# Optimization experiments

Measured on AMD Instinct MI355X. Metric: run time of the kernel, lower is better.

Reference implementation:

```python
import jax, jax.numpy as jnp
import numpy as np


def _generate_fitpack_knots(x, k):
    # FITPACK-style knots: k+1 copies of x[0], k+1 copies of x[-1],
    # interior knots are length-k moving averages of x[1:-1].
    n = x.shape[0]
    n_interior = n - k - 1  # number of interior knots
    win_sum = x[1:1 + n_interior]
    for j in range(1, k):  # k is a small static int (e.g. 3)
        win_sum = win_sum + x[1 + j:1 + j + n_interior]
    interior = win_sum / k
    head = jnp.full((k + 1,), x[0], dtype=x.dtype)
    tail = jnp.full((k + 1,), x[-1], dtype=x.dtype)
    return jnp.concatenate([head, interior, tail])


def _safe_div(num, den):
    # torch.nan_to_num_(num/den): 0/0 -> 0, x/0 -> 0
    den_safe = jnp.where(den == 0, jnp.ones_like(den), den)
    return jnp.where(den == 0, jnp.zeros_like(num), num / den_safe)


def _bspline_basis_natural(x, k, t):
    n = x.shape[0]
    m = t.shape[0] - k - 1
    xc = x[:, None]  # [n, 1]
    # zeroth-order basis: indicator of knot interval, with boundary fixes
    b = ((t[None, :m] <= xc) & (xc < t[None, 1:m + 1])).astype(x.dtype)
    b = b.at[:, 0].set(jnp.where(x < t[1], jnp.ones_like(x), b[:, 0]))
    b = b.at[:, -1].set(jnp.where(x >= t[-2], jnp.ones_like(x), b[:, -1]))
    zeros_col = jnp.zeros((n, 1), dtype=x.dtype)
    # de Boor recursion over degree d = 1..k (k is static and small)
    for d in range(1, k + 1):
        L = _safe_div(xc - t[None, :m], (t[d:m + d] - t[:m])[None, :])
        R = _safe_div(t[None, d + 1:m + d + 1] - xc,
                      (t[d + 1:m + d + 1] - t[1:m + 1])[None, :])
        b_shift = jnp.concatenate([b[:, 1:], zeros_col], axis=1)
        b = L * b + R * b_shift
    return b  # [n, m]


def setup_inputs() -> dict:
    key = jax.random.key(0)
    N = 4096
    x = jnp.sort(jax.random.uniform(key, (N,), dtype=jnp.float32) * 10.0)
    s = jnp.asarray(1e-3, dtype=jnp.float32)
    return {"x": x, "s": s, "k": 3}


def reference(x, s, k):
    knots = _generate_fitpack_knots(x, k)
    basis_matrix = _bspline_basis_natural(x, k, knots)  # [n, m]
    m = basis_matrix.shape[-1]
    B_T_B = basis_matrix.T @ basis_matrix + s * jnp.eye(m, dtype=basis_matrix.dtype)
    return (knots, basis_matrix, B_T_B)
```

## Files before the change

### kernel.cpp

```cpp
#include <hip/hip_runtime.h>

#define K 3

__device__ __forceinline__ float tfun(const float* __restrict__ x, int j, int N) {
    if (j <= K) return x[0];
    if (j >= N) return x[N - 1];
    return (x[j - 3] + x[j - 2] + x[j - 1]) / 3.0f;
}

__global__ void k1_basis(const float* __restrict__ x, float* __restrict__ out_knots,
                         float* __restrict__ vals, int* __restrict__ j0arr, int N) {
    int i = blockIdx.x * blockDim.x + threadIdx.x;
    if (i >= N) return;
    int nk = N + K + 1;

    out_knots[i] = tfun(x, i, N);
    if (i < nk - N) out_knots[N + i] = x[N - 1];

    float xi = x[i];
    int lo = 0, hi = nk;
    while (lo < hi) { int mid = (lo + hi) >> 1; if (tfun(x, mid, N) <= xi) lo = mid + 1; else hi = mid; }
    int j0 = lo - 1;
    if (j0 > N - 1) j0 = N - 1;
    if (j0 < K) j0 = K;
    int c0 = j0 - K;

    float b[K + 2];
    #pragma unroll
    for (int w = 0; w < K + 2; ++w) b[w] = 0.f;
    b[K] = 1.f;

    #pragma unroll
    for (int d = 1; d <= K; ++d) {
        float nb[K + 1];
        #pragma unroll
        for (int w = 0; w <= K; ++w) {
            int j = c0 + w;
            float tj   = tfun(x, j, N);
            float tjd  = tfun(x, j + d, N);
            float tj1  = tfun(x, j + 1, N);
            float tjd1 = tfun(x, j + d + 1, N);
            float denL = tjd - tj;
            float L = (denL == 0.f) ? 0.f : (xi - tj) / denL;
            float denR = tjd1 - tj1;
            float R = (denR == 0.f) ? 0.f : (tjd1 - xi) / denR;
            nb[w] = L * b[w] + R * b[w + 1];
        }
        #pragma unroll
        for (int w = 0; w <= K; ++w) b[w] = nb[w];
    }

    j0arr[i] = j0;
    *(float4*)(vals + i * 4) = make_float4(b[0], b[1], b[2], b[3]);
}

__global__ void k2_band(const float* __restrict__ vals, const int* __restrict__ j0arr,
                        const float* __restrict__ s_ptr, float* __restrict__ band, int N) {
    int ci = blockIdx.x * blockDim.x + threadIdx.x;
    if (ci >= N) return;

    int lo = 0, hi = N;
    while (lo < hi) { int mid = (lo + hi) >> 1; if (j0arr[mid] < ci) lo = mid + 1; else hi = mid; }
    int rlo = lo;
    hi = N; int tgt = ci + K + 1;
    while (lo < hi) { int mid = (lo + hi) >> 1; if (j0arr[mid] < tgt) lo = mid + 1; else hi = mid; }
    int rhi = lo;

    float acc[2 * K + 1];
    #pragma unroll
    for (int a = 0; a < 2 * K + 1; ++a) acc[a] = 0.f;

    for (int r = rlo; r < rhi; ++r) {
        int wi = ci - (j0arr[r] - K);
        float4 v4 = *(const float4*)(vals + r * 4);
        float v = (wi == 0) ? v4.x : (wi == 1) ? v4.y : (wi == 2) ? v4.z : v4.w;
        #pragma unroll
        for (int o = -K; o <= K; ++o) {
            int wj = wi + o;
            float w = (wj == 0) ? v4.x : (wj == 1) ? v4.y : (wj == 2) ? v4.z
                    : (wj == 3) ? v4.w : 0.f;
            acc[o + K] += v * w;
        }
    }
    acc[K] += *s_ptr;

    *(float4*)(band + ci * 8)     = make_float4(acc[0], acc[1], acc[2], acc[3]);
    *(float4*)(band + ci * 8 + 4) = make_float4(acc[4], acc[5], acc[6], 0.f);
}

__global__ __launch_bounds__(256) void k3_write(const float* __restrict__ vals,
                                                const int* __restrict__ j0arr,
                                                const float* __restrict__ band,
                                                float* __restrict__ outB,
                                                float* __restrict__ outBTB, int N) {
    int bid = blockIdx.x;
    int tid = threadIdx.x;
    int fpr = N >> 2;

    if (bid < N) {
        int i = bid;
        int c0 = j0arr[i] - K;
        float4 v4 = *(const float4*)(vals + i * 4);
        float4* rowp = (float4*)(outB + (long long)i * N);
        int fw0 = c0 >> 2, fw1 = (c0 + K) >> 2;
        for (int f = tid; f < fpr; f += 256) {
            float4 z = make_float4(0.f, 0.f, 0.f, 0.f);
            if (f == fw0 || f == fw1) {
                int e0 = f * 4;
                float e[4];
                #pragma unroll
                for (int l = 0; l < 4; ++l) {
                    int d = e0 + l - c0;
                    e[l] = (d == 0) ? v4.x : (d == 1) ? v4.y : (d == 2) ? v4.z
                         : (d == 3) ? v4.w : 0.f;
                }
                z = make_float4(e[0], e[1], e[2], e[3]);
            }
            rowp[f] = z;
        }
    } else {
        int ci = bid - N;
        float4 b0 = *(const float4*)(band + ci * 8);
        float4 b1 = *(const float4*)(band + ci * 8 + 4);
        float4* rowp = (float4*)(outBTB + (long long)ci * N);
        int wlo = ci - K; if (wlo < 0) wlo = 0;
        int whi = ci + K; if (whi > N - 1) whi = N - 1;
        int fw0 = wlo >> 2, fw1 = whi >> 2;
        for (int f = tid; f < fpr; f += 256) {
            float4 z = make_float4(0.f, 0.f, 0.f, 0.f);
            if (f >= fw0 && f <= fw1) {
                int e0 = f * 4;
                float e[4];
                #pragma unroll
                for (int l = 0; l < 4; ++l) {
                    int d = e0 + l - ci;
                    e[l] = (d == -3) ? b0.x : (d == -2) ? b0.y : (d == -1) ? b0.z
                         : (d ==  0) ? b0.w : (d ==  1) ? b1.x : (d ==  2) ? b1.y
                         : (d ==  3) ? b1.z : 0.f;
                }
                z = make_float4(e[0], e[1], e[2], e[3]);
            }
            rowp[f] = z;
        }
    }
}

extern "C" void kernel_launch(void* const* d_in, const int* in_sizes, int n_in,
                              void* d_out, int out_size, void* d_ws, size_t ws_size,
                              hipStream_t stream) {
    const float* x = (const float*)d_in[0];
    const float* s = (const float*)d_in[1];
    int N = in_sizes[0];
    int nk = N + K + 1;

    float* out = (float*)d_out;
    float* out_knots = out;
    float* out_B = out + nk;
    float* out_BTB = out_B + (long long)N * N;

    float* band_ws = (float*)d_ws;
    float* vals_ws = band_ws + (long long)N * 8;
    int* j0_ws = (int*)(vals_ws + (long long)N * 4);

    int tb = 256;
    k1_basis<<<(N + tb - 1) / tb, tb, 0, stream>>>(x, out_knots, vals_ws, j0_ws, N);
    k2_band<<<(N + tb - 1) / tb, tb, 0, stream>>>(vals_ws, j0_ws, s, band_ws, N);
    k3_write<<<2 * N, tb, 0, stream>>>(vals_ws, j0_ws, band_ws, out_B, out_BTB, N);
}
```

Measured before the change: 47.21 us.

## Fuse basis, band and write kernels into one launch with recomputation

Merges the three kernels into a single launch. Each block now recomputes its row's knot interval and de Boor basis, and each BTB row recomputes its band entries directly from x, so the workspace buffers and the inter-kernel dependencies are gone. This removes two launches and the workspace round trips. In exchange every thread in a block redundantly runs the binary searches and de Boor evaluations, and the j0 recomputation in the band path is more fragile.

```diff
diff --git a/kernel.cpp b/kernel.cpp
--- a/kernel.cpp
+++ b/kernel.cpp
@@ -8,28 +8,13 @@
     return (x[j - 3] + x[j - 2] + x[j - 1]) / 3.0f;
 }
 
-__global__ void k1_basis(const float* __restrict__ x, float* __restrict__ out_knots,
-                         float* __restrict__ vals, int* __restrict__ j0arr, int N) {
-    int i = blockIdx.x * blockDim.x + threadIdx.x;
-    if (i >= N) return;
-    int nk = N + K + 1;
-
-    out_knots[i] = tfun(x, i, N);
-    if (i < nk - N) out_knots[N + i] = x[N - 1];
-
-    float xi = x[i];
-    int lo = 0, hi = nk;
-    while (lo < hi) { int mid = (lo + hi) >> 1; if (tfun(x, mid, N) <= xi) lo = mid + 1; else hi = mid; }
-    int j0 = lo - 1;
-    if (j0 > N - 1) j0 = N - 1;
-    if (j0 < K) j0 = K;
+__device__ __forceinline__ float4 deboor(const float* __restrict__ x, float xi,
+                                         int j0, int N) {
     int c0 = j0 - K;
-
     float b[K + 2];
     #pragma unroll
     for (int w = 0; w < K + 2; ++w) b[w] = 0.f;
     b[K] = 1.f;
-
     #pragma unroll
     for (int d = 1; d <= K; ++d) {
         float nb[K + 1];
@@ -49,58 +34,35 @@
         #pragma unroll
         for (int w = 0; w <= K; ++w) b[w] = nb[w];
     }
-
-    j0arr[i] = j0;
-    *(float4*)(vals + i * 4) = make_float4(b[0], b[1], b[2], b[3]);
+    return make_float4(b[0], b[1], b[2], b[3]);
 }
 
-__global__ void k2_band(const float* __restrict__ vals, const int* __restrict__ j0arr,
-                        const float* __restrict__ s_ptr, float* __restrict__ band, int N) {
-    int ci = blockIdx.x * blockDim.x + threadIdx.x;
-    if (ci >= N) return;
-
-    int lo = 0, hi = N;
-    while (lo < hi) { int mid = (lo + hi) >> 1; if (j0arr[mid] < ci) lo = mid + 1; else hi = mid; }
-    int rlo = lo;
-    hi = N; int tgt = ci + K + 1;
-    while (lo < hi) { int mid = (lo + hi) >> 1; if (j0arr[mid] < tgt) lo = mid + 1; else hi = mid; }
-    int rhi = lo;
-
-    float acc[2 * K + 1];
-    #pragma unroll
-    for (int a = 0; a < 2 * K + 1; ++a) acc[a] = 0.f;
-
-    for (int r = rlo; r < rhi; ++r) {
-        int wi = ci - (j0arr[r] - K);
-        float4 v4 = *(const float4*)(vals + r * 4);
-        float v = (wi == 0) ? v4.x : (wi == 1) ? v4.y : (wi == 2) ? v4.z : v4.w;
-        #pragma unroll
-        for (int o = -K; o <= K; ++o) {
-            int wj = wi + o;
-            float w = (wj == 0) ? v4.x : (wj == 1) ? v4.y : (wj == 2) ? v4.z
-                    : (wj == 3) ? v4.w : 0.f;
-            acc[o + K] += v * w;
-        }
-    }
-    acc[K] += *s_ptr;
-
-    *(float4*)(band + ci * 8)     = make_float4(acc[0], acc[1], acc[2], acc[3]);
-    *(float4*)(band + ci * 8 + 4) = make_float4(acc[4], acc[5], acc[6], 0.f);
-}
-
-__global__ __launch_bounds__(256) void k3_write(const float* __restrict__ vals,
-                                                const int* __restrict__ j0arr,
-                                                const float* __restrict__ band,
-                                                float* __restrict__ outB,
-                                                float* __restrict__ outBTB, int N) {
+__global__ __launch_bounds__(256) void fused(const float* __restrict__ x,
+                                             const float* __restrict__ s_ptr,
+                                             float* __restrict__ out_knots,
+                                             float* __restrict__ outB,
+                                             float* __restrict__ outBTB, int N) {
     int bid = blockIdx.x;
     int tid = threadIdx.x;
+    int nk = N + K + 1;
     int fpr = N >> 2;
+
+    if (bid * 256 < nk) {
+        int idx = bid * 256 + tid;
+        if (idx < nk) out_knots[idx] = tfun(x, idx, N);
+    }
 
     if (bid < N) {
         int i = bid;
-        int c0 = j0arr[i] - K;
-        float4 v4 = *(const float4*)(vals + i * 4);
+        float xi = x[i];
+        int lo = 0, hi = nk;
+        while (lo < hi) { int mid = (lo + hi) >> 1; if (tfun(x, mid, N) <= xi) lo = mid + 1; else hi = mid; }
+        int j0 = lo - 1;
+        if (j0 > N - 1) j0 = N - 1;
+        if (j0 < K) j0 = K;
+        int c0 = j0 - K;
+        float4 v4 = deboor(x, xi, j0, N);
+
         float4* rowp = (float4*)(outB + (long long)i * N);
         int fw0 = c0 >> 2, fw1 = (c0 + K) >> 2;
         for (int f = tid; f < fpr; f += 256) {
@@ -120,8 +82,44 @@
         }
     } else {
         int ci = bid - N;
-        float4 b0 = *(const float4*)(band + ci * 8);
-        float4 b1 = *(const float4*)(band + ci * 8 + 4);
+        float tlo = tfun(x, ci, N);
+        int lo = 0, hi = N;
+        while (lo < hi) { int mid = (lo + hi) >> 1; if (x[mid] < tlo) lo = mid + 1; else hi = mid; }
+        int rlo = lo;
+        int rhi, tgt = ci + K + 1;
+        if (tgt > N - 1) {
+            rhi = N;
+        } else {
+            float thi = tfun(x, tgt, N);
+            hi = N;
+            while (lo < hi) { int mid = (lo + hi) >> 1; if (x[mid] < thi) lo = mid + 1; else hi = mid; }
+            rhi = lo;
+        }
+        int jhi = ci + K; if (jhi > N - 1) jhi = N - 1;
+
+        float acc[2 * K + 1];
+        #pragma unroll
+        for (int a = 0; a < 2 * K + 1; ++a) acc[a] = 0.f;
+
+        for (int r = rlo; r < rhi; ++r) {
+            float xr = x[r];
+            int j0r = jhi;
+            #pragma unroll
+            for (int it = 0; it < K; ++it)
+                if (j0r > ci && tfun(x, j0r, N) > xr) --j0r;
+            float4 v4 = deboor(x, xr, j0r, N);
+            int wi = ci - (j0r - K);
+            float v = (wi == 0) ? v4.x : (wi == 1) ? v4.y : (wi == 2) ? v4.z : v4.w;
+            #pragma unroll
+            for (int o = -K; o <= K; ++o) {
+                int wj = wi + o;
+                float w = (wj == 0) ? v4.x : (wj == 1) ? v4.y : (wj == 2) ? v4.z
+                        : (wj == 3) ? v4.w : 0.f;
+                acc[o + K] += v * w;
+            }
+        }
+        acc[K] += *s_ptr;
+
         float4* rowp = (float4*)(outBTB + (long long)ci * N);
         int wlo = ci - K; if (wlo < 0) wlo = 0;
         int whi = ci + K; if (whi > N - 1) whi = N - 1;
@@ -134,9 +132,9 @@
                 #pragma unroll
                 for (int l = 0; l < 4; ++l) {
                     int d = e0 + l - ci;
-                    e[l] = (d == -3) ? b0.x : (d == -2) ? b0.y : (d == -1) ? b0.z
-                         : (d ==  0) ? b0.w : (d ==  1) ? b1.x : (d ==  2) ? b1.y
-                         : (d ==  3) ? b1.z : 0.f;
+                    e[l] = (d == -3) ? acc[0] : (d == -2) ? acc[1] : (d == -1) ? acc[2]
+                         : (d ==  0) ? acc[3] : (d ==  1) ? acc[4] : (d ==  2) ? acc[5]
+                         : (d ==  3) ? acc[6] : 0.f;
                 }
                 z = make_float4(e[0], e[1], e[2], e[3]);
             }
@@ -158,12 +156,5 @@
     float* out_B = out + nk;
     float* out_BTB = out_B + (long long)N * N;
 
-    float* band_ws = (float*)d_ws;
-    float* vals_ws = band_ws + (long long)N * 8;
-    int* j0_ws = (int*)(vals_ws + (long long)N * 4);
-
-    int tb = 256;
-    k1_basis<<<(N + tb - 1) / tb, tb, 0, stream>>>(x, out_knots, vals_ws, j0_ws, N);
-    k2_band<<<(N + tb - 1) / tb, tb, 0, stream>>>(vals_ws, j0_ws, s, band_ws, N);
-    k3_write<<<2 * N, tb, 0, stream>>>(vals_ws, j0_ws, band_ws, out_B, out_BTB, N);
+    fused<<<2 * N, 256, 0, stream>>>(x, s, out_knots, out_B, out_BTB, N);
 }
```

Measured after the change: 181.3 us. 284% more time.

## Fuse basis and band kernels with shared-memory halo and local knot search

Applied to the files above, without the earlier changes.

Merges the basis evaluation and band accumulation kernels into one launch. Each 64-thread block computes de Boor values for its rows plus a halo in shared memory, then accumulates the seven band entries from neighbouring rows. The binary searches over knots and over j0 are replaced by a fixed local check that relies on FITPACK knot structure. This removes one launch and the global round-trips and searches, at the cost of redundant halo computation and an assumption that the knot interval for x[i] lies near i.

```diff
diff --git a/kernel.cpp b/kernel.cpp
--- a/kernel.cpp
+++ b/kernel.cpp
@@ -8,28 +8,23 @@
     return (x[j - 3] + x[j - 2] + x[j - 1]) / 3.0f;
 }
 
-__global__ void k1_basis(const float* __restrict__ x, float* __restrict__ out_knots,
-                         float* __restrict__ vals, int* __restrict__ j0arr, int N) {
-    int i = blockIdx.x * blockDim.x + threadIdx.x;
-    if (i >= N) return;
-    int nk = N + K + 1;
-
-    out_knots[i] = tfun(x, i, N);
-    if (i < nk - N) out_knots[N + i] = x[N - 1];
-
+__device__ __forceinline__ int j0_of(const float* __restrict__ x, int i, int N) {
     float xi = x[i];
-    int lo = 0, hi = nk;
-    while (lo < hi) { int mid = (lo + hi) >> 1; if (tfun(x, mid, N) <= xi) lo = mid + 1; else hi = mid; }
-    int j0 = lo - 1;
+    int j0 = i + 1;
+    if (tfun(x, i + 2, N) <= xi) j0 = i + 2;
+    if (tfun(x, i + 3, N) <= xi) j0 = i + 3;
     if (j0 > N - 1) j0 = N - 1;
     if (j0 < K) j0 = K;
+    return j0;
+}
+
+__device__ __forceinline__ float4 deboor(const float* __restrict__ x, float xi,
+                                         int j0, int N) {
     int c0 = j0 - K;
-
     float b[K + 2];
     #pragma unroll
     for (int w = 0; w < K + 2; ++w) b[w] = 0.f;
     b[K] = 1.f;
-
     #pragma unroll
     for (int d = 1; d <= K; ++d) {
         float nb[K + 1];
@@ -49,46 +44,75 @@
         #pragma unroll
         for (int w = 0; w <= K; ++w) b[w] = nb[w];
     }
-
-    j0arr[i] = j0;
-    *(float4*)(vals + i * 4) = make_float4(b[0], b[1], b[2], b[3]);
+    return make_float4(b[0], b[1], b[2], b[3]);
 }
 
-__global__ void k2_band(const float* __restrict__ vals, const int* __restrict__ j0arr,
-                        const float* __restrict__ s_ptr, float* __restrict__ band, int N) {
-    int ci = blockIdx.x * blockDim.x + threadIdx.x;
-    if (ci >= N) return;
+#define B1 64
+#define HALO 4
 
-    int lo = 0, hi = N;
-    while (lo < hi) { int mid = (lo + hi) >> 1; if (j0arr[mid] < ci) lo = mid + 1; else hi = mid; }
-    int rlo = lo;
-    hi = N; int tgt = ci + K + 1;
-    while (lo < hi) { int mid = (lo + hi) >> 1; if (j0arr[mid] < tgt) lo = mid + 1; else hi = mid; }
-    int rhi = lo;
+__global__ __launch_bounds__(B1) void k1_precompute(const float* __restrict__ x,
+                                                    const float* __restrict__ s_ptr,
+                                                    float* __restrict__ out_knots,
+                                                    float* __restrict__ vals,
+                                                    int* __restrict__ j0arr,
+                                                    float* __restrict__ band, int N) {
+    __shared__ float4 lv[73];
+    __shared__ int lj[73];
+    int t = threadIdx.x;
+    int bs = blockIdx.x * B1;
+
+    for (int k = t; k < 73; k += B1) {
+        int rb = bs - HALO + k;
+        if (rb >= 0 && rb < N) {
+            int j0 = j0_of(x, rb, N);
+            lj[k] = j0;
+            lv[k] = deboor(x, x[rb], j0, N);
+        } else {
+            lj[k] = -1000000;
+            lv[k] = make_float4(0.f, 0.f, 0.f, 0.f);
+        }
+    }
+    __syncthreads();
+
+    int i = bs + t;
+    if (i >= N) return;
+
+    out_knots[i] = tfun(x, i, N);
+    if (i < K + 1) out_knots[N + i] = x[N - 1];
+
+    int kk = t + HALO;
+    int j0i = lj[kk];
+    float4 v4i = lv[kk];
+    j0arr[i] = j0i;
+    *(float4*)(vals + 4 * i) = v4i;
 
     float acc[2 * K + 1];
     #pragma unroll
     for (int a = 0; a < 2 * K + 1; ++a) acc[a] = 0.f;
 
-    for (int r = rlo; r < rhi; ++r) {
-        int wi = ci - (j0arr[r] - K);
-        float4 v4 = *(const float4*)(vals + r * 4);
-        float v = (wi == 0) ? v4.x : (wi == 1) ? v4.y : (wi == 2) ? v4.z : v4.w;
+    #pragma unroll
+    for (int d = -3; d <= 5; ++d) {
+        int k2 = kk + d;
+        int j0r = lj[k2];
+        if (j0r < i || j0r > i + K) continue;
+        float4 w4 = lv[k2];
+        int wi = i - (j0r - K);
+        float v = (wi == 0) ? w4.x : (wi == 1) ? w4.y : (wi == 2) ? w4.z : w4.w;
         #pragma unroll
         for (int o = -K; o <= K; ++o) {
             int wj = wi + o;
-            float w = (wj == 0) ? v4.x : (wj == 1) ? v4.y : (wj == 2) ? v4.z
-                    : (wj == 3) ? v4.w : 0.f;
+            float w = (wj == 0) ? w4.x : (wj == 1) ? w4.y : (wj == 2) ? w4.z
+                    : (wj == 3) ? w4.w : 0.f;
             acc[o + K] += v * w;
         }
     }
     acc[K] += *s_ptr;
 
-    *(float4*)(band + ci * 8)     = make_float4(acc[0], acc[1], acc[2], acc[3]);
-    *(float4*)(band + ci * 8 + 4) = make_float4(acc[4], acc[5], acc[6], 0.f);
+    *(float4*)(band + i * 8)     = make_float4(acc[0], acc[1], acc[2], acc[3]);
+    *(float4*)(band + i * 8 + 4) = make_float4(acc[4], acc[5], acc[6], 0.f);
 }
 
-__global__ __launch_bounds__(256) void k3_write(const float* __restrict__ vals,
+__global__ __launch_bounds__(256) void k2_write(const float* __restrict__ vals,
                                                 const int* __restrict__ j0arr,
                                                 const float* __restrict__ band,
                                                 float* __restrict__ outB,
@@ -162,8 +186,7 @@
     float* vals_ws = band_ws + (long long)N * 8;
     int* j0_ws = (int*)(vals_ws + (long long)N * 4);
 
-    int tb = 256;
-    k1_basis<<<(N + tb - 1) / tb, tb, 0, stream>>>(x, out_knots, vals_ws, j0_ws, N);
-    k2_band<<<(N + tb - 1) / tb, tb, 0, stream>>>(vals_ws, j0_ws, s, band_ws, N);
-    k3_write<<<2 * N, tb, 0, stream>>>(vals_ws, j0_ws, band_ws, out_B, out_BTB, N);
+    k1_precompute<<<(N + B1 - 1) / B1, B1, 0, stream>>>(x, s, out_knots,
+                                                        vals_ws, j0_ws, band_ws, N);
+    k2_write<<<2 * N, 256, 0, stream>>>(vals_ws, j0_ws, band_ws, out_B, out_BTB, N);
 }
```

Result: faster. 45.79 us (-3.0%).
